# Optimization experiments

Hardware: AMD Instinct MI355X
Metric: run time of the kernel (lower is better)

Reference implementation:

```python
import jax, jax.numpy as jnp
import numpy as np

B, C, K, V, S = 16384, 1024, 128, 256, 6
HM, HG, M = 512, 384, 1024
LB = 2
GATE_DIM = C + K + 2 * V + 5  # 1669
CADENCE = 8.0
TEMP = 0.25
REFRESH_T, SPAWN_T, PROMOTE_T, RETIRE_T = 0.55, 0.60, 0.50, 0.15
DECAY = 0.995
EPS_N = 1e-6


def _mlp(x, W1, b1, W2, b2):
    return jax.nn.gelu(x @ W1 + b1, approximate=False) @ W2 + b2


def _l2norm(x):
    n = jnp.linalg.norm(x, axis=-1, keepdims=True)
    return x / jnp.maximum(n, EPS_N)


def setup_inputs():
    key = jax.random.key(0)
    ks = jax.random.split(key, 16)
    p = lambda k, sh: (0.02 * jax.random.normal(k, sh)).astype(jnp.float32)
    return {
        "context": jax.random.normal(ks[0], (B, C), jnp.float32),
        "ledger_bias": jax.random.normal(ks[1], (B, LB), jnp.float32),
        "keys": jax.random.normal(ks[2], (B, S, K), jnp.float32),
        "values": jax.random.normal(ks[3], (B, S, V), jnp.float32),
        "confidence": jax.random.uniform(ks[4], (B, S, 1), jnp.float32),
        "age": 16.0 * jax.random.uniform(ks[5], (B, S, 1), jnp.float32),
        "alive": (jax.random.uniform(ks[6], (B, S, 1)) > 0.3).astype(jnp.float32),
        "Wk1": p(ks[7], (C, HM)), "bk1": jnp.zeros(HM, jnp.float32),
        "Wk2": p(ks[8], (HM, K)), "bk2": jnp.zeros(K, jnp.float32),
        "Wv1": p(ks[9], (C, HM)), "bv1": jnp.zeros(HM, jnp.float32),
        "Wv2": p(ks[10], (HM, V)), "bv2": jnp.zeros(V, jnp.float32),
        "Wg1": p(ks[11], (4, GATE_DIM, HG)), "bg1": jnp.zeros((4, HG), jnp.float32),
        "Wg2": p(ks[12], (4, HG, 1)), "bg2": jnp.zeros((4, 1), jnp.float32),
        "Wsum": p(ks[13], (V, M)), "bsum": jnp.zeros(M, jnp.float32),
        "g_ln": jnp.ones(M, jnp.float32), "b_ln": jnp.zeros(M, jnp.float32),
    }


def _forward(context, ledger_bias, keys, values, confidence, age, alive,
             Wk1, bk1, Wk2, bk2, Wv1, bv1, Wv2, bv2,
             Wg1, bg1, Wg2, bg2, Wsum, bsum, g_ln, b_ln):
    cand_key = _l2norm(_mlp(context, Wk1, bk1, Wk2, bk2))   # [B,K]
    cand_val = _mlp(context, Wv1, bv1, Wv2, bv2)            # [B,V]
    # --- slot match: cosine similarity over live slots, gather best ---
    live = alive[..., 0] > 0                                # [B,S]
    safe_keys = _l2norm(keys + (1.0 - alive) * 1e-4)
    scores = jnp.einsum("bd,bsd->bs", cand_key, safe_keys)
    scores = jnp.where(live, scores, -1e4)
    has_live = jnp.any(live, axis=1, keepdims=True)         # [B,1]
    best_score = jnp.where(has_live, scores.max(axis=1, keepdims=True), 0.0)
    best_index = jnp.where(has_live, jnp.argmax(scores, axis=1, keepdims=True), 0)
    matched_val = jnp.take_along_axis(values, best_index[:, :, None], axis=1)[:, 0]
    matched_age = jnp.take_along_axis(age, best_index[:, :, None], axis=1)[:, 0]
    cadence_prior = jax.nn.sigmoid((matched_age - CADENCE) / CADENCE)
    surprise = 1.0 - best_score
    feats = jnp.concatenate([context, cand_key, cand_val, matched_val,
                             best_score, cadence_prior, surprise, ledger_bias], axis=-1)
    # --- four gate MLPs fused into one batched einsum ---
    h = jax.nn.gelu(jnp.einsum("bf,gfh->bgh", feats, Wg1) + bg1, approximate=False)
    probs = jax.nn.sigmoid(jnp.einsum("bgh,gho->bgo", h, Wg2) + bg2)[:, :, 0]  # [B,4]
    refresh_p, spawn_p, promote_p, retire_p = (probs[:, i:i + 1] for i in range(4))
    # --- soft masks (hard=False path) ---
    has_live_f = alive.max(axis=1)                          # [B,1]
    t = max(TEMP, 1e-4)
    refresh_raw = jax.nn.sigmoid((refresh_p - REFRESH_T) / t) * has_live_f
    spawn_raw = jax.nn.sigmoid((spawn_p - SPAWN_T) / t)
    denom = 1.0 + refresh_raw + spawn_raw
    refresh = refresh_raw / denom
    spawn = spawn_raw / denom
    promote = jax.nn.sigmoid((promote_p - PROMOTE_T) / t)
    retire = jax.nn.sigmoid((retire_p - RETIRE_T) / t)
    # --- spawn slot selection ---
    inactive = (alive[..., 0] < 0.5).astype(jnp.float32)
    has_inactive = inactive.max(axis=1, keepdims=True) > 0.5
    inactive_choice = jnp.argmax(inactive, axis=1, keepdims=True)
    utility = (confidence - 0.01 * age)[..., 0]
    utility = jnp.where(best_index == jnp.arange(S)[None, :], 1e4, utility)
    spawn_index = jnp.where(has_inactive, inactive_choice,
                            jnp.argmin(utility, axis=1, keepdims=True))
    # --- masked scatter update into slot memory ---
    match_hot = jax.nn.one_hot(best_index[:, 0], S, dtype=keys.dtype)[:, :, None]
    spawn_hot = jax.nn.one_hot(spawn_index[:, 0], S, dtype=keys.dtype)[:, :, None]
    refresh_slot = match_hot * refresh[:, None, :]
    spawn_slot = spawn_hot * spawn[:, None, :]
    retire_slot = match_hot * retire[:, None, :]
    write = jnp.clip(refresh_slot + spawn_slot, 0.0, 1.0)
    keys_n = keys * (1.0 - write) + write * cand_key[:, None, :]
    values_n = values * (1.0 - write) + write * cand_val[:, None, :]
    conf_n = (confidence * DECAY * (1.0 - write) + write) * (1.0 - retire_slot)
    age_n = (age + alive) * (1.0 - write)
    alive_n = jnp.clip(alive * (1.0 - retire_slot) + write, 0.0, 1.0)
    # --- confidence-weighted summary + promoted memory token ---
    w = alive_n * conf_n
    summary = (values_n * w).sum(axis=1) / (w.sum(axis=1) + EPS_N)  # [B,V]
    z = summary @ Wsum + bsum
    mu = z.mean(axis=-1, keepdims=True)
    var = ((z - mu) ** 2).mean(axis=-1, keepdims=True)
    promoted = promote * (((z - mu) / jnp.sqrt(var + 1e-5)) * g_ln + b_ln)
    return promoted, summary, keys_n, values_n, conf_n, age_n, alive_n


def reference(context, ledger_bias, keys, values, confidence, age, alive,
              Wk1, bk1, Wk2, bk2, Wv1, bv1, Wv2, bv2,
              Wg1, bg1, Wg2, bg2, Wsum, bsum, g_ln, b_ln):
    return _forward(context, ledger_bias, keys, values, confidence, age, alive,
                    Wk1, bk1, Wk2, bk2, Wv1, bv1, Wv2, bv2,
                    Wg1, bg1, Wg2, bg2, Wsum, bsum, g_ln, b_ln)
```

## Files before the change

kernel.cpp:

```cpp
#include <hip/hip_runtime.h>
#include <math.h>

static constexpr int Bsz  = 16384;
static constexpr int Cdim = 1024;
static constexpr int Kdim = 128;
static constexpr int Vdim = 256;
static constexpr int HMd  = 512;
static constexpr int GOUTd= 1536;
static constexpr int GDIM = 1669;
static constexpr int GPAD = 1728;
static constexpr int F2D  = 704;
static constexpr int Mdim = 1024;
static constexpr float TAU = 2e-3f;

typedef __attribute__((ext_vector_type(8))) _Float16 f16x8;
typedef __attribute__((ext_vector_type(4))) _Float16 f16x4;
typedef __attribute__((ext_vector_type(4))) float f32x4;

__device__ __forceinline__ float sigm(float x){ return 1.0f/(1.0f+__expf(-x)); }
__device__ __forceinline__ float gelu(float x){
    float y = 0.70710678118654752440f * x;
    float a = fabsf(y);
    float t1 = __builtin_amdgcn_rcpf(fmaf(0.3275911f, a, 1.0f));
    float p = t1*fmaf(t1, fmaf(t1, fmaf(t1, fmaf(t1, 1.061405429f, -1.453152027f),
                                         1.421413741f), -0.284496736f), 0.254829592f);
    float e = __expf(-a*a);
    float er = fmaf(-p, e, 1.0f);
    er = (y < 0.0f) ? -er : er;
    return 0.5f*x*(1.0f+er);
}
__device__ __forceinline__ ushort f2h(float f){
    return __builtin_bit_cast(ushort, (_Float16)f);
}


__global__ __launch_bounds__(256) void k_zero(int* p){ if (threadIdx.x==0) *p = 0; }

__global__ __launch_bounds__(256) void k_cat(float* __restrict__ dst,
        const float* __restrict__ a, const float* __restrict__ b, int na, int ntot){
    int i = blockIdx.x*256 + threadIdx.x;
    if (i >= ntot) return;
    dst[i] = (i < na) ? a[i] : b[i-na];
}

__global__ __launch_bounds__(256) void k_wt(const float* __restrict__ W,
                                            ushort* __restrict__ Wt, int K, int N){
    __shared__ float tile[64][65];
    int n0 = blockIdx.x*64, k0 = blockIdx.y*64;
    int tx = threadIdx.x & 63, ty = threadIdx.x >> 6;
    #pragma unroll
    for (int i=0;i<64;i+=4)
        tile[ty+i][tx] = W[(size_t)(k0+ty+i)*N + n0 + tx];
    __syncthreads();
    #pragma unroll
    for (int i=0;i<64;i+=4)
        Wt[(size_t)(n0+ty+i)*K + k0 + tx] = f2h(tile[tx][ty+i]);
}

__global__ __launch_bounds__(256) void k_wg1t(const float* __restrict__ Wg1,
                                              ushort* __restrict__ Wt){
    __shared__ float tile[64][65];
    int g = blockIdx.z;
    int h0 = blockIdx.x*64, f0 = blockIdx.y*64;
    int tx = threadIdx.x & 63, ty = threadIdx.x >> 6;
    #pragma unroll
    for (int i=0;i<64;i+=4){
        int f = f0+ty+i;
        tile[ty+i][tx] = (f < GDIM) ? Wg1[((size_t)g*GDIM+f)*384 + h0+tx] : 0.0f;
    }
    __syncthreads();
    #pragma unroll
    for (int i=0;i<64;i+=4)
        Wt[((size_t)(g*384 + h0+ty+i))*GPAD + f0+tx] = f2h(tile[tx][ty+i]);
}

__global__ __launch_bounds__(256) void k_cvt(const float* __restrict__ x,
                                             ushort* __restrict__ y, size_t n4){
    size_t i = (size_t)blockIdx.x*256 + threadIdx.x;
    if (i >= n4) return;
    float4 v = ((const float4*)x)[i];
    ushort4 o = { f2h(v.x), f2h(v.y), f2h(v.z), f2h(v.w) };
    ((ushort4*)y)[i] = o;
}

__device__ __forceinline__ void gload_lds16(const void* g, void* l){
    typedef __attribute__((address_space(1))) const unsigned gu32;
    typedef __attribute__((address_space(3))) unsigned lu32;
    __builtin_amdgcn_global_load_lds((gu32*)(unsigned long long)g,
                                     (lu32*)(unsigned)(unsigned long long)l,
                                     16, 0, 0);
}

template<int ACT, int OUTM, int SRC, int NX>
__global__ __launch_bounds__(256) void k_mgemm(const ushort* __restrict__ A,
        const ushort* __restrict__ A2, const ushort* __restrict__ Bt,
        const float* __restrict__ bias, const float* __restrict__ Wg2,
        void* __restrict__ Cout, int K, int lda){
    __shared__ alignas(16) ushort lds[32768];
    int t = threadIdx.x;
    int l = t & 63, w = t >> 6;
    int wm = w >> 1, wn = w & 1;
    int nwg = NX * (int)gridDim.y;
    int orig = (int)blockIdx.y * NX + (int)blockIdx.x;
    int qq = nwg >> 3, rr = nwg & 7;
    int xcd = orig & 7, loc = orig >> 3;
    int wgid = (xcd < rr ? xcd*(qq+1) : rr*(qq+1) + (xcd-rr)*qq) + loc;
    int bx = wgid % NX;
    int by = wgid / NX;
    size_t row0 = (size_t)by * 128;
    int col0 = bx * 128;
    constexpr int N = NX*128;
    f32x4 acc[4][4] = {};
    int lrow = l >> 3;
    int lc8  = (l & 7) ^ lrow;
    int nt = K >> 6;

    auto stage = [&](int buf, int k0){
        const ushort* Ag; int astr; int koff;
        if (SRC == 1){
            if (k0 < 1024){ Ag = A;  astr = 1024; koff = k0; }
            else          { Ag = A2; astr = F2D;  koff = k0 - 1024; }
        } else if (SRC == 2){
            Ag = A; astr = lda; koff = k0 + (bx ? 512 : 0);
        } else { Ag = A; astr = lda; koff = k0; }
        ushort* As = lds + buf*16384;
        ushort* Bs = As + 8192;
        #pragma unroll
        for (int i = 0; i < 4; ++i){
            int ch = w*4 + i;
            int r  = ch*8 + lrow;
            gload_lds16(Ag + (row0 + r)*(size_t)astr + koff + lc8*8, As + ch*512);
            gload_lds16(Bt + (size_t)(col0 + r)*K + k0 + lc8*8, Bs + ch*512);
        }
    };
    auto compute = [&](int buf){
        const ushort* As = lds + buf*16384;
        const ushort* Bs = As + 8192;
        #pragma unroll
        for (int kk = 0; kk < 2; ++kk){
            f16x8 af[4], bfr[4];
            int j8 = kk*4 + (l >> 4);
            #pragma unroll
            for (int m = 0; m < 4; ++m){
                int row = wm*64 + m*16 + (l & 15);
                int c16 = j8 ^ (row & 7);
                af[m] = *(const f16x8*)(const void*)(As + row*64 + c16*8);
            }
            #pragma unroll
            for (int n = 0; n < 4; ++n){
                int rowb = wn*64 + n*16 + (l & 15);
                int c16 = j8 ^ (rowb & 7);
                bfr[n] = *(const f16x8*)(const void*)(Bs + rowb*64 + c16*8);
            }
            #pragma unroll
            for (int m = 0; m < 4; ++m)
                #pragma unroll
                for (int n = 0; n < 4; ++n)
                    acc[m][n] = __builtin_amdgcn_mfma_f32_16x16x32_f16(af[m], bfr[n], acc[m][n], 0, 0, 0);
        }
    };

    stage(0, 0);
    for (int tt = 0; tt < nt-1; ++tt){
        __builtin_amdgcn_s_barrier();
        stage((tt+1)&1, (tt+1)<<6);
        asm volatile("s_waitcnt vmcnt(8)" ::: "memory");
        __builtin_amdgcn_s_barrier();
        compute(tt&1);
    }
    asm volatile("s_waitcnt vmcnt(0)" ::: "memory");
    __builtin_amdgcn_s_barrier();
    compute((nt-1)&1);

    int q = l >> 4, cf = l & 15;
    if (OUTM == 2){
        __syncthreads();
        float* sacc = (float*)lds;
        if (t < 128) sacc[t] = 0.f;
        __syncthreads();
        #pragma unroll
        for (int m = 0; m < 4; ++m){
            #pragma unroll
            for (int i = 0; i < 4; ++i){
                float v = 0.f;
                #pragma unroll
                for (int n = 0; n < 4; ++n){
                    int col = col0 + wn*64 + n*16 + cf;
                    float z = acc[m][n][i] + bias[col];
                    v += gelu(z) * Wg2[col];
                }
                atomicAdd(&sacc[wm*64 + m*16 + q*4 + i], v);
            }
        }
        __syncthreads();
        if (t < 128) ((float*)Cout)[(row0 + t)*NX + bx] = sacc[t];
    } else {
        #pragma unroll
        for (int m = 0; m < 4; ++m){
            #pragma unroll
            for (int n = 0; n < 4; ++n){
                int col = col0 + wn*64 + n*16 + cf;
                float bv = bias[col];
                #pragma unroll
                for (int i = 0; i < 4; ++i){
                    size_t r = row0 + wm*64 + m*16 + q*4 + i;
                    float v = acc[m][n][i] + bv;
                    if (ACT == 1) v = gelu(v);
                    if (OUTM == 1) ((ushort*)Cout)[r*N + col] = f2h(v);
                    else           ((float*) Cout)[r*N + col] = v;
                }
            }
        }
    }
}

template<int ACT>
__global__ __launch_bounds__(256) void k_gemm_dyn(const float* __restrict__ A,
                                                  const float* __restrict__ W,
                                                  const float* __restrict__ bias,
                                                  float* __restrict__ C,
                                                  const int* __restrict__ cntp,
                                                  int N, int K){
    int M = (*cntp + 63) & ~63;
    size_t row0 = (size_t)blockIdx.y * 64;
    if ((int)row0 >= M) return;
    __shared__ float As[32][68];
    __shared__ float Ws[32][64];
    int t  = threadIdx.x;
    int tx = t & 15, ty = t >> 4;
    int col0 = blockIdx.x * 64;
    float acc[4][4] = {};
    int ra = t >> 3;
    int ca = (t & 7) << 2;
    int rw = t >> 4;
    int cw = (t & 15) << 2;
    for (int k0 = 0; k0 < K; k0 += 32){
        float4 a0 = *(const float4*)(A + (row0 + ra)*K + k0 + ca);
        float4 a1 = *(const float4*)(A + (row0 + ra + 32)*K + k0 + ca);
        float4 w0 = *(const float4*)(W + (size_t)(k0 + rw)*N + col0 + cw);
        float4 w1 = *(const float4*)(W + (size_t)(k0 + rw + 16)*N + col0 + cw);
        As[ca+0][ra] = a0.x; As[ca+1][ra] = a0.y; As[ca+2][ra] = a0.z; As[ca+3][ra] = a0.w;
        As[ca+0][ra+32] = a1.x; As[ca+1][ra+32] = a1.y; As[ca+2][ra+32] = a1.z; As[ca+3][ra+32] = a1.w;
        *(float4*)&Ws[rw][cw]    = w0;
        *(float4*)&Ws[rw+16][cw] = w1;
        __syncthreads();
        #pragma unroll
        for (int kk = 0; kk < 32; ++kk){
            float4 av = *(const float4*)&As[kk][ty*4];
            float4 wv = *(const float4*)&Ws[kk][tx*4];
            float a4[4] = {av.x, av.y, av.z, av.w};
            float w4[4] = {wv.x, wv.y, wv.z, wv.w};
            #pragma unroll
            for (int i=0;i<4;i++)
                #pragma unroll
                for (int j=0;j<4;j++)
                    acc[i][j] = fmaf(a4[i], w4[j], acc[i][j]);
        }
        __syncthreads();
    }
    #pragma unroll
    for (int i=0;i<4;i++){
        size_t r = row0 + ty*4 + i;
        #pragma unroll
        for (int j=0;j<4;j++){
            int c = col0 + tx*4 + j;
            float v = acc[i][j] + bias[c];
            if (ACT == 1) v = gelu(v);
            C[r*N + c] = v;
        }
    }
}

__global__ __launch_bounds__(256) void k_gather(const float* __restrict__ ctx,
        const int* __restrict__ flaglist, const int* __restrict__ flagcnt,
        float* __restrict__ fctx, int b0){
    int i = (blockIdx.x<<2) + (threadIdx.x>>6);
    int lane = threadIdx.x & 63;
    int cnt = *flagcnt;
    int cntpad = (cnt + 63) & ~63;
    if (i >= cntpad) return;
    float4* dst = (float4*)(fctx + (size_t)i*1024);
    if (i < cnt){
        const float4* src = (const float4*)(ctx + ((size_t)b0 + flaglist[i])*1024);
        #pragma unroll
        for (int j=0;j<4;j++) dst[lane + 64*j] = src[lane + 64*j];
    } else {
        float4 z = {0.f,0.f,0.f,0.f};
        #pragma unroll
        for (int j=0;j<4;j++) dst[lane + 64*j] = z;
    }
}

__global__ __launch_bounds__(256) void k_fixapply(const float* __restrict__ fck,
        const float* __restrict__ keys, const float* __restrict__ values,
        const float* __restrict__ age,  const float* __restrict__ alive,
        float* __restrict__ ckc, ushort* __restrict__ feats2, int* __restrict__ bidx,
        const int* __restrict__ flagcnt, const int* __restrict__ flaglist, int b0){
    int i = (blockIdx.x<<2) + (threadIdx.x>>6);
    int lane = threadIdx.x & 63;
    if (i >= *flagcnt) return;
    int w = flaglist[i];
    size_t b = (size_t)b0 + w;
    float2 c2 = ((const float2*)(fck + (size_t)i*128))[lane];
    float ss = c2.x*c2.x + c2.y*c2.y;
    #pragma unroll
    for (int o=32;o;o>>=1) ss += __shfl_xor(ss,o);
    float inv = 1.0f / fmaxf(sqrtf(ss), 1e-6f);
    float2 cc; cc.x = c2.x*inv; cc.y = c2.y*inv;
    ((float2*)(ckc + (size_t)w*128))[lane] = cc;
    ushort* f2 = feats2 + (size_t)w*F2D;
    { ushort2 o = { f2h(cc.x), f2h(cc.y) };
      ((ushort2*)f2)[lane] = o; }
    float s1v = -1e30f; int bi = 0; int anylive = 0;
    #pragma unroll
    for (int s=0;s<6;s++){
        float a = alive[b*6+s];
        float2 k2 = ((const float2*)(keys + (b*6+s)*128))[lane];
        float ks = k2.x*k2.x + k2.y*k2.y;
        float dt = cc.x*k2.x + cc.y*k2.y;
        #pragma unroll
        for (int o=32;o;o>>=1){ ks += __shfl_xor(ks,o); dt += __shfl_xor(dt,o); }
        float sc;
        if (a > 0.0f){ sc = dt / fmaxf(sqrtf(ks), 1e-6f); anylive = 1; }
        else sc = -1e4f;
        if (sc > s1v){ s1v = sc; bi = s; }
    }
    int bis = anylive ? bi : 0;
    float bsc = anylive ? s1v : 0.0f;
    float4 mv = ((const float4*)(values + (b*6+bis)*256))[lane];
    ushort4 mo = { f2h(mv.x), f2h(mv.y), f2h(mv.z), f2h(mv.w) };
    ((ushort4*)(f2+384))[lane] = mo;
    if (lane == 0){
        bidx[w] = bis;
        float mage = age[b*6 + bis];
        f2[640] = f2h(bsc);
        f2[641] = f2h(sigm((mage - 8.0f)*0.125f));
        f2[642] = f2h(1.0f - bsc);
    }
}

__global__ __launch_bounds__(256) void k_feats(
        const float* __restrict__ ledger, const float* __restrict__ keys,
        const float* __restrict__ values, const float* __restrict__ age,
        const float* __restrict__ alive,  const float* __restrict__ ckv,
        float* __restrict__ ckc, ushort* __restrict__ feats2,
        int* __restrict__ bidx, int* __restrict__ flagcnt, int* __restrict__ flaglist,
        int b0){
    int w = (blockIdx.x<<2) + (threadIdx.x>>6);
    int lane = threadIdx.x & 63;
    size_t b = (size_t)b0 + w;
    const float* ckr = ckv + (size_t)w*384;
    float2 cr2 = ((const float2*)ckr)[lane];
    float ssc = cr2.x*cr2.x + cr2.y*cr2.y;
    #pragma unroll
    for (int o=32;o;o>>=1) ssc += __shfl_xor(ssc,o);
    float invc = 1.0f / fmaxf(sqrtf(ssc), 1e-6f);
    float2 cc; cc.x = cr2.x*invc; cc.y = cr2.y*invc;
    ((float2*)(ckc + (size_t)w*128))[lane] = cc;
    float s1v = -1e30f, s2v = -1e30f; int bi = 0; int anylive = 0;
    #pragma unroll
    for (int s=0;s<6;s++){
        float a = alive[b*6+s];
        float2 k2 = ((const float2*)(keys + (b*6+s)*128))[lane];
        float ss = k2.x*k2.x + k2.y*k2.y;
        float dt = cc.x*k2.x + cc.y*k2.y;
        #pragma unroll
        for (int o=32;o;o>>=1){ ss += __shfl_xor(ss,o); dt += __shfl_xor(dt,o); }
        float sc;
        if (a > 0.0f){ sc = dt / fmaxf(sqrtf(ss), 1e-6f); anylive = 1; }
        else sc = -1e4f;
        if (sc > s1v){ s2v = s1v; s1v = sc; bi = s; }
        else if (sc > s2v) s2v = sc;
    }
    float best_score = anylive ? s1v : 0.0f;
    int bis = anylive ? bi : 0;
    if (lane == 0 && (s1v - s2v) < TAU){
        int pos = atomicAdd(flagcnt, 1);
        flaglist[pos] = w;
    }
    float4 mv = ((const float4*)(values + (b*6+bis)*256))[lane];
    float mage = age[b*6+bis];
    float cad = sigm((mage - 8.0f)*0.125f);
    ushort* f2 = feats2 + (size_t)w*F2D;
    { ushort2 o = { f2h(cc.x), f2h(cc.y) };
      ((ushort2*)f2)[lane] = o; }
    { float4 v = ((const float4*)(ckr+128))[lane];
      ushort4 o = { f2h(v.x), f2h(v.y), f2h(v.z), f2h(v.w) };
      ((ushort4*)(f2+128))[lane] = o; }
    { ushort4 o = { f2h(mv.x), f2h(mv.y), f2h(mv.z), f2h(mv.w) };
      ((ushort4*)(f2+384))[lane] = o; }
    if (lane == 0){
        f2[640] = f2h(best_score);
        f2[641] = f2h(cad);
        f2[642] = f2h(1.0f - best_score);
        f2[643] = f2h(ledger[b*2]);
        f2[644] = f2h(ledger[b*2+1]);
        bidx[w] = bis;
    }
    if (lane < GPAD - GDIM) f2[645+lane] = 0;
}

__global__ __launch_bounds__(256) void k_update(const float* __restrict__ keys,
        const float* __restrict__ values, const float* __restrict__ conf,
        const float* __restrict__ age,    const float* __restrict__ alive,
        const float* __restrict__ ckC,    const float* __restrict__ ckv,
        const float* __restrict__ part,   const float* __restrict__ bg2,
        const int* __restrict__ bidx,
        float* __restrict__ probsC,
        float* __restrict__ o_keys, float* __restrict__ o_vals,
        float* __restrict__ o_conf, float* __restrict__ o_age,
        float* __restrict__ o_aliv, float* __restrict__ o_sum,
        ushort* __restrict__ o_sumb, int b0){
    int w = (blockIdx.x<<2) + (threadIdx.x>>6);
    int lane = threadIdx.x & 63;
    size_t b = (size_t)b0 + w;
    const float* pp = part + (size_t)w*12;
    float pb[4];
    #pragma unroll
    for (int g=0; g<4; ++g)
        pb[g] = sigm(pp[3*g] + pp[3*g+1] + pp[3*g+2] + bg2[g]);
    if (lane < 4) probsC[w*4 + lane] = pb[lane];
    float rp = pb[0], sp = pb[1], tp = pb[3];
    float al[6], cf[6], ag[6];
    float hl = 0.f;
    #pragma unroll
    for (int s=0;s<6;s++){
        al[s]=alive[b*6+s]; cf[s]=conf[b*6+s]; ag[s]=age[b*6+s];
        hl = fmaxf(hl, al[s]);
    }
    float rr = hl * sigm((rp-0.55f)*4.0f);
    float sr = sigm((sp-0.60f)*4.0f);
    float den = 1.0f + rr + sr;
    float refresh = rr/den, spawn = sr/den;
    float retire = sigm((tp-0.15f)*4.0f);
    int bi = bidx[w];
    int ic = -1;
    #pragma unroll
    for (int s=5;s>=0;s--) if (al[s] < 0.5f) ic = s;
    int si;
    if (ic >= 0) si = ic;
    else {
        float bu = 1e30f; int am = 0;
        #pragma unroll
        for (int s=0;s<6;s++){
            float u = (s == bi) ? 1e4f : (cf[s] - 0.01f*ag[s]);
            if (u < bu){ bu = u; am = s; }
        }
        si = am;
    }
    float2 cc  = ((const float2*)(ckC + (size_t)w*128))[lane];
    float4 cvv = ((const float4*)(ckv + (size_t)w*384 + 128))[lane];
    float s0=0,s1=0,s2=0,s3=0, wsum=0;
    #pragma unroll
    for (int s=0;s<6;s++){
        float wr = refresh*(s==bi ? 1.0f:0.0f) + spawn*(s==si ? 1.0f:0.0f);
        wr = fminf(wr, 1.0f);
        float rs = (s==bi) ? retire : 0.0f;
        float om = 1.0f - wr;
        float2 k2 = ((const float2*)(keys + (b*6+s)*128))[lane];
        float2 kn; kn.x = k2.x*om + wr*cc.x; kn.y = k2.y*om + wr*cc.y;
        ((float2*)(o_keys + (b*6+s)*128))[lane] = kn;
        float4 vv = ((const float4*)(values + (b*6+s)*256))[lane];
        float4 vn;
        vn.x = vv.x*om + wr*cvv.x; vn.y = vv.y*om + wr*cvv.y;
        vn.z = vv.z*om + wr*cvv.z; vn.w = vv.w*om + wr*cvv.w;
        ((float4*)(o_vals + (b*6+s)*256))[lane] = vn;
        float cn  = (cf[s]*0.995f*om + wr) * (1.0f - rs);
        float an  = fminf(fmaxf(al[s]*(1.0f - rs) + wr, 0.0f), 1.0f);
        float agn = (ag[s] + al[s]) * om;
        float wgt = an * cn;
        wsum += wgt;
        s0 += vn.x*wgt; s1 += vn.y*wgt; s2 += vn.z*wgt; s3 += vn.w*wgt;
        if (lane == s){ o_conf[b*6+s] = cn; o_age[b*6+s] = agn; o_aliv[b*6+s] = an; }
    }
    float inv = 1.0f/(wsum + 1e-6f);
    float4 sm; sm.x = s0*inv; sm.y = s1*inv; sm.z = s2*inv; sm.w = s3*inv;
    ((float4*)(o_sum + b*256))[lane] = sm;
    ushort4 sb = { f2h(sm.x), f2h(sm.y), f2h(sm.z), f2h(sm.w) };
    ((ushort4*)(o_sumb + (size_t)w*256))[lane] = sb;
}

__global__ __launch_bounds__(256) void k_ln(const ushort* __restrict__ z,
        const float* __restrict__ probs, const float* __restrict__ g_ln,
        const float* __restrict__ b_ln,  float* __restrict__ o_prom, int b0){
    int w = blockIdx.x; int t = threadIdx.x;
    int lane = t & 63, wid = t >> 6;
    f16x4 hv = ((const f16x4*)(z + (size_t)w*1024))[t];
    float v0 = (float)hv[0], v1 = (float)hv[1], v2 = (float)hv[2], v3 = (float)hv[3];
    float s = v0+v1+v2+v3;
    #pragma unroll
    for (int o=32;o;o>>=1) s += __shfl_xor(s,o);
    __shared__ float red[4];
    if (lane==0) red[wid] = s;
    __syncthreads();
    float mu = (red[0]+red[1]+red[2]+red[3]) * (1.0f/1024.0f);
    float d0=v0-mu, d1=v1-mu, d2=v2-mu, d3=v3-mu;
    float ss = d0*d0+d1*d1+d2*d2+d3*d3;
    #pragma unroll
    for (int o=32;o;o>>=1) ss += __shfl_xor(ss,o);
    __syncthreads();
    if (lane==0) red[wid] = ss;
    __syncthreads();
    float var = (red[0]+red[1]+red[2]+red[3]) * (1.0f/1024.0f);
    float rstd = 1.0f / sqrtf(var + 1e-5f);
    float pm = sigm((probs[w*4+2]-0.50f)*4.0f);
    float4 g  = ((const float4*)g_ln)[t];
    float4 bb = ((const float4*)b_ln)[t];
    float4 o;
    o.x = pm*(d0*rstd*g.x + bb.x);
    o.y = pm*(d1*rstd*g.y + bb.y);
    o.z = pm*(d2*rstd*g.z + bb.z);
    o.w = pm*(d3*rstd*g.w + bb.w);
    ((float4*)(o_prom + ((size_t)b0 + w)*1024))[t] = o;
}

extern "C" void kernel_launch(void* const* d_in, const int* in_sizes, int n_in,
                              void* d_out, int out_size, void* d_ws, size_t ws_size,
                              hipStream_t stream){
    const float* ctx    = (const float*)d_in[0];
    const float* ledger = (const float*)d_in[1];
    const float* keys   = (const float*)d_in[2];
    const float* values = (const float*)d_in[3];
    const float* conf   = (const float*)d_in[4];
    const float* age    = (const float*)d_in[5];
    const float* alive  = (const float*)d_in[6];
    const float* Wk1 = (const float*)d_in[7];  const float* bk1 = (const float*)d_in[8];
    const float* Wk2 = (const float*)d_in[9];  const float* bk2 = (const float*)d_in[10];
    const float* Wv1 = (const float*)d_in[11]; const float* bv1 = (const float*)d_in[12];
    const float* Wv2 = (const float*)d_in[13]; const float* bv2 = (const float*)d_in[14];
    const float* Wg1 = (const float*)d_in[15]; const float* bg1 = (const float*)d_in[16];
    const float* Wg2 = (const float*)d_in[17]; const float* bg2 = (const float*)d_in[18];
    const float* Wsum= (const float*)d_in[19]; const float* bsum= (const float*)d_in[20];
    const float* g_ln= (const float*)d_in[21]; const float* b_ln= (const float*)d_in[22];

    float* out   = (float*)d_out;
    float* o_prom= out;
    float* o_sum = o_prom + (size_t)Bsz*Mdim;
    float* o_keys= o_sum  + (size_t)Bsz*Vdim;
    float* o_vals= o_keys + (size_t)Bsz*6*Kdim;
    float* o_conf= o_vals + (size_t)Bsz*6*Vdim;
    float* o_age = o_conf + (size_t)Bsz*6;
    float* o_aliv= o_age  + (size_t)Bsz*6;

    char* p = (char*)d_ws;
    auto alloc = [&](size_t bytes)->char*{
        char* r = p; p += (bytes + 255) & ~(size_t)255; return r;
    };
    ushort* ctxh  = (ushort*)alloc((size_t)Bsz*Cdim*2);
    ushort* W1m   = (ushort*)alloc((size_t)1024*Cdim*2);
    ushort* W2m   = (ushort*)alloc((size_t)384*HMd*2);
    ushort* Wg1tt = (ushort*)alloc((size_t)GOUTd*GPAD*2);
    ushort* Wsumt = (ushort*)alloc((size_t)Mdim*Vdim*2);
    float*  biasm1= (float*) alloc(1024*4);
    float*  biasm2= (float*) alloc(384*4);
    size_t fixed = (size_t)(p - (char*)d_ws);
    size_t per_row = 2048  + 1536  + 512  + 1408
                   + 48  + 4096  + 512  + 16
                   + 4 + 4 + 2048  + 512  + 128 ;
    int CB = 16384;
    while (CB > 128 && fixed + (size_t)CB*per_row + 16384 > ws_size) CB >>= 1;
    ushort* H      = (ushort*)alloc((size_t)CB*1024*2);
    float*  ckv    = (float*) alloc((size_t)CB*384*4);
    float*  ckc    = (float*) alloc((size_t)CB*Kdim*4);
    ushort* feats2 = (ushort*)alloc((size_t)CB*F2D*2);
    float*  part   = (float*) alloc((size_t)CB*12*4);
    float*  zbuf   = (float*) alloc((size_t)CB*Mdim*4);
    ushort* sumb   = (ushort*)alloc((size_t)CB*Vdim*2);
    float*  probsC = (float*) alloc((size_t)CB*4*4);
    int*    bidxC  = (int*)   alloc((size_t)CB*4);
    int*    flagl  = (int*)   alloc((size_t)CB*4);
    int*    flagc  = (int*)   alloc(256);
    float*  fH     = (float*) alloc((size_t)CB*HMd*4);
    float*  fck    = (float*) alloc((size_t)CB*Kdim*4);
    float*  fctx   = zbuf;
    ushort* zh     = (ushort*)zbuf;

    dim3 blk(256);
    k_cvt<<<(int)(((size_t)Bsz*Cdim/4 + 255)/256), blk, 0, stream>>>(ctx, ctxh, (size_t)Bsz*Cdim/4);
    k_wt<<<dim3(HMd/64,  Cdim/64), blk, 0, stream>>>(Wk1, W1m,             Cdim, HMd);
    k_wt<<<dim3(HMd/64,  Cdim/64), blk, 0, stream>>>(Wv1, W1m + 512*Cdim,  Cdim, HMd);
    k_wt<<<dim3(Kdim/64, HMd/64),  blk, 0, stream>>>(Wk2, W2m,             HMd, Kdim);
    k_wt<<<dim3(Vdim/64, HMd/64),  blk, 0, stream>>>(Wv2, W2m + 128*HMd,   HMd, Vdim);
    k_wt<<<dim3(Mdim/64, Vdim/64), blk, 0, stream>>>(Wsum, Wsumt, Vdim, Mdim);
    k_wg1t<<<dim3(384/64, GPAD/64, 4), blk, 0, stream>>>(Wg1, Wg1tt);
    k_cat<<<(1024+255)/256, blk, 0, stream>>>(biasm1, bk1, bv1, 512, 1024);
    k_cat<<<(384+255)/256,  blk, 0, stream>>>(biasm2, bk2, bv2, 128, 384);

    for (int b0 = 0; b0 < Bsz; b0 += CB){
        k_zero<<<1, blk, 0, stream>>>(flagc);
        k_mgemm<1,1,0,8><<<dim3(8, CB/128), blk, 0, stream>>>(
            ctxh + (size_t)b0*Cdim, nullptr, W1m, biasm1, nullptr, H, Cdim, Cdim);
        k_mgemm<0,0,2,3><<<dim3(3, CB/128), blk, 0, stream>>>(
            H, nullptr, W2m, biasm2, nullptr, ckv, HMd, 1024);
        k_feats<<<CB/4, blk, 0, stream>>>(ledger, keys, values, age, alive,
                                          ckv, ckc, feats2, bidxC, flagc, flagl, b0);
        k_gather<<<CB/4, blk, 0, stream>>>(ctx, flagl, flagc, fctx, b0);
        k_gemm_dyn<1><<<dim3(HMd/64,  CB/64), blk, 0, stream>>>(fctx, Wk1, bk1, fH,  flagc, HMd,  Cdim);
        k_gemm_dyn<0><<<dim3(Kdim/64, CB/64), blk, 0, stream>>>(fH,   Wk2, bk2, fck, flagc, Kdim, HMd);
        k_fixapply<<<CB/4, blk, 0, stream>>>(fck, keys, values, age, alive,
                                             ckc, feats2, bidxC, flagc, flagl, b0);
        k_mgemm<0,2,1,12><<<dim3(12, CB/128), blk, 0, stream>>>(
            ctxh + (size_t)b0*Cdim, feats2, Wg1tt, bg1, Wg2, part, GPAD, 0);
        k_update<<<CB/4, blk, 0, stream>>>(keys, values, conf, age, alive, ckc, ckv,
                                           part, bg2, bidxC, probsC,
                                           o_keys, o_vals, o_conf, o_age, o_aliv,
                                           o_sum, sumb, b0);
        k_mgemm<0,1,0,8><<<dim3(8, CB/128), blk, 0, stream>>>(
            sumb, nullptr, Wsumt, bsum, nullptr, zh, Vdim, Vdim);
        k_ln<<<CB, blk, 0, stream>>>(zh, probsC, g_ln, b_ln, o_prom, b0);
    }
}
```

Baseline: 471.3 us.

## Add 256x256-tile 8-wave MFMA GEMM with quadrant ping-pong for large GEMMs

Adds a new GEMM kernel that uses 256x256 output tiles, 512 threads, 128KB of dynamic LDS and one block per CU. It stages A and B in half-tile pieces interleaved with four quadrant MFMA phases and raises wave priority (s_setprio) around the MFMA phases. The first-layer MLP, gate and summary GEMMs switch to it, which is meant to raise arithmetic intensity per LDS and global load. The gate epilogue now writes two partial sums per 256-column block, and the update kernel remaps those 12 partials to the 4 gates. The risks are lower occupancy, fewer workgroups per GEMM, and reliance on large dynamic LDS allocations.

Measured after the change: 647.6 us. 37.4% more time.

```diff
diff --git a/kernel.cpp b/kernel.cpp
--- a/kernel.cpp
+++ b/kernel.cpp
@@ -89,6 +89,198 @@
     __builtin_amdgcn_global_load_lds((gu32*)(unsigned long long)g,
                                      (lu32*)(unsigned)(unsigned long long)l,
                                      16, 0, 0);
+}
+
+template<int QM, int QN>
+__device__ __forceinline__ void do_mfma(f32x4 (&acc)[2][2][4][2],
+                                        const f16x8 (&afr)[4][2], const f16x8 (&bfr)[2][2]){
+    #pragma unroll
+    for (int kk=0;kk<2;kk++)
+        #pragma unroll
+        for (int mi=0;mi<4;mi++)
+            #pragma unroll
+            for (int ni=0;ni<2;ni++)
+                acc[QM][QN][mi][ni] = __builtin_amdgcn_mfma_f32_16x16x32_f16(
+                    afr[mi][kk], bfr[ni][kk], acc[QM][QN][mi][ni], 0, 0, 0);
+}
+
+__device__ __forceinline__ void load_afr(const ushort* ldsu, int pt, int qm,
+                                         int wr2, int l, f16x8 (&afr)[4][2]){
+    const ushort* Ah = ldsu + ((pt<<1)|qm)*8192;
+    #pragma unroll
+    for (int mi=0;mi<4;mi++){
+        int row = wr2*64 + mi*16 + (l & 15);
+        #pragma unroll
+        for (int kk=0;kk<2;kk++)
+            afr[mi][kk] = *(const f16x8*)(const void*)(Ah + row*64 + (((kk*4+(l>>4))^(row&7))<<3));
+    }
+}
+__device__ __forceinline__ void load_bfr(const ushort* ldsu, int pt, int qn,
+                                         int wc4, int l, f16x8 (&bfr)[2][2]){
+    const ushort* Bh = ldsu + 32768 + ((pt<<1)|qn)*8192;
+    #pragma unroll
+    for (int ni=0;ni<2;ni++){
+        int col = wc4*32 + ni*16 + (l & 15);
+        #pragma unroll
+        for (int kk=0;kk<2;kk++)
+            bfr[ni][kk] = *(const f16x8*)(const void*)(Bh + col*64 + (((kk*4+(l>>4))^(col&7))<<3));
+    }
+}
+
+template<int ACT, int OUTM, int SRC, int NX>
+__global__ __launch_bounds__(512, 1) void k_mgemm256(const ushort* __restrict__ A,
+        const ushort* __restrict__ A2, const ushort* __restrict__ Bt,
+        const float* __restrict__ bias, const float* __restrict__ Wg2,
+        void* __restrict__ Cout, int K, int lda){
+    extern __shared__ char smem[];
+    ushort* ldsu = (ushort*)smem;
+    int t = threadIdx.x;
+    int l = t & 63, wv = t >> 6;
+    int wr2 = wv >> 2, wc4 = wv & 3;
+    int nwg = NX * (int)gridDim.y;
+    int orig = (int)blockIdx.y * NX + (int)blockIdx.x;
+    int qq = nwg >> 3, rr = nwg & 7;
+    int xcd = orig & 7, loc = orig >> 3;
+    int wgid = (xcd < rr ? xcd*(qq+1) : rr*(qq+1) + (xcd-rr)*qq) + loc;
+    int bx = wgid % NX;
+    int by = wgid / NX;
+    size_t row0 = (size_t)by * 256;
+    int col0 = bx * 256;
+    constexpr int N = NX*256;
+    int nt = K >> 6;
+
+    f32x4 acc[2][2][4][2] = {};
+    f16x8 afr[4][2], bfr[2][2];
+    int lrow = l >> 3;
+    int lc8s = ((l & 7) ^ lrow) << 3;
+
+    auto stage_half = [&](int h){
+        if (h >= 4*nt) return;
+        int k  = h & 3;
+        int tau = h >> 2;
+        int p  = tau & 1;
+        int k0 = tau << 6;
+        if (k == 0 || k == 3){
+            int hn = (k == 3);
+            ushort* dst = ldsu + 32768 + ((p<<1)|hn)*8192;
+            size_t rbase = (size_t)col0 + hn*128;
+            #pragma unroll
+            for (int i=0;i<2;i++){
+                int ch = i*8 + wv;
+                int r  = ch*8 + lrow;
+                gload_lds16(Bt + (rbase + r)*(size_t)K + k0 + lc8s, dst + ch*512);
+            }
+        } else {
+            int hm = (k == 1);
+            ushort* dst = ldsu + ((p<<1)|hm)*8192;
+            const ushort* Ag; size_t astr; int koff;
+            if (SRC == 1){
+                if (k0 < 1024){ Ag = A;  astr = 1024; koff = k0; }
+                else          { Ag = A2; astr = F2D;  koff = k0 - 1024; }
+            } else { Ag = A; astr = (size_t)lda; koff = k0; }
+            size_t rbase = row0 + (size_t)hm*128;
+            #pragma unroll
+            for (int i=0;i<2;i++){
+                int ch = i*8 + wv;
+                int r  = ch*8 + lrow;
+                gload_lds16(Ag + (rbase + r)*astr + koff + lc8s, dst + ch*512);
+            }
+        }
+    };
+
+    for (int h = 0; h < 6; ++h) stage_half(h);
+    asm volatile("s_waitcnt vmcnt(4)" ::: "memory");
+    __builtin_amdgcn_s_barrier();
+
+    for (int tt = 0; tt < nt; ++tt){
+        int pt = tt & 1;
+        int hb = 4*tt + 6;
+        load_afr(ldsu, pt, 0, wr2, l, afr);
+        load_bfr(ldsu, pt, 0, wc4, l, bfr);
+        stage_half(hb+0);
+        __builtin_amdgcn_s_barrier();
+        __builtin_amdgcn_s_setprio(1);
+        do_mfma<0,0>(acc, afr, bfr);
+        __builtin_amdgcn_s_setprio(0);
+        __builtin_amdgcn_s_barrier();
+        load_afr(ldsu, pt, 1, wr2, l, afr);
+        stage_half(hb+1);
+        __builtin_amdgcn_s_barrier();
+        __builtin_amdgcn_s_setprio(1);
+        do_mfma<1,0>(acc, afr, bfr);
+        __builtin_amdgcn_s_setprio(0);
+        __builtin_amdgcn_s_barrier();
+        load_bfr(ldsu, pt, 1, wc4, l, bfr);
+        stage_half(hb+2);
+        __builtin_amdgcn_s_barrier();
+        __builtin_amdgcn_s_setprio(1);
+        do_mfma<1,1>(acc, afr, bfr);
+        __builtin_amdgcn_s_setprio(0);
+        __builtin_amdgcn_s_barrier();
+        load_afr(ldsu, pt, 0, wr2, l, afr);
+        stage_half(hb+3);
+        __builtin_amdgcn_s_barrier();
+        __builtin_amdgcn_s_setprio(1);
+        do_mfma<0,1>(acc, afr, bfr);
+        __builtin_amdgcn_s_setprio(0);
+        if (tt == nt-2) asm volatile("s_waitcnt vmcnt(0)" ::: "memory");
+        else            asm volatile("s_waitcnt vmcnt(4)" ::: "memory");
+        __builtin_amdgcn_s_barrier();
+    }
+
+    int q4 = l >> 4, cf = l & 15;
+    if (OUTM == 2){
+        __syncthreads();
+        float* sacc = (float*)ldsu;
+        sacc[t] = 0.f;
+        __syncthreads();
+        int g_lo = col0 / 384;
+        #pragma unroll
+        for (int qm=0;qm<2;qm++)
+        #pragma unroll
+        for (int qn=0;qn<2;qn++)
+        #pragma unroll
+        for (int mi=0;mi<4;mi++)
+        #pragma unroll
+        for (int ni=0;ni<2;ni++){
+            int col_l = qn*128 + wc4*32 + ni*16 + cf;
+            int colg  = col0 + col_l;
+            int slot  = (colg/384 == g_lo) ? 0 : 1;
+            float wg  = Wg2[colg];
+            float bv  = bias[colg];
+            #pragma unroll
+            for (int i=0;i<4;i++){
+                int row_l = qm*128 + wr2*64 + mi*16 + q4*4 + i;
+                float z = acc[qm][qn][mi][ni][i] + bv;
+                atomicAdd(&sacc[row_l*2 + slot], gelu(z)*wg);
+            }
+        }
+        __syncthreads();
+        if (t < 256){
+            ((float*)Cout)[(row0 + t)*(NX*2) + bx*2 + 0] = sacc[t*2];
+            ((float*)Cout)[(row0 + t)*(NX*2) + bx*2 + 1] = sacc[t*2+1];
+        }
+    } else {
+        #pragma unroll
+        for (int qm=0;qm<2;qm++)
+        #pragma unroll
+        for (int qn=0;qn<2;qn++)
+        #pragma unroll
+        for (int mi=0;mi<4;mi++)
+        #pragma unroll
+        for (int ni=0;ni<2;ni++){
+            int col = col0 + qn*128 + wc4*32 + ni*16 + cf;
+            float bv = bias[col];
+            #pragma unroll
+            for (int i=0;i<4;i++){
+                size_t r = row0 + qm*128 + wr2*64 + mi*16 + q4*4 + i;
+                float v = acc[qm][qn][mi][ni][i] + bv;
+                if (ACT == 1) v = gelu(v);
+                if (OUTM == 1) ((ushort*)Cout)[r*N + col] = f2h(v);
+                else           ((float*) Cout)[r*N + col] = v;
+            }
+        }
+    }
 }
 
 template<int ACT, int OUTM, int SRC, int NX>
@@ -116,20 +308,17 @@
     int nt = K >> 6;
 
     auto stage = [&](int buf, int k0){
-        const ushort* Ag; int astr; int koff;
-        if (SRC == 1){
-            if (k0 < 1024){ Ag = A;  astr = 1024; koff = k0; }
-            else          { Ag = A2; astr = F2D;  koff = k0 - 1024; }
-        } else if (SRC == 2){
-            Ag = A; astr = lda; koff = k0 + (bx ? 512 : 0);
-        } else { Ag = A; astr = lda; koff = k0; }
+        const ushort* Ag; size_t astr; int koff;
+        if (SRC == 2){
+            Ag = A; astr = (size_t)lda; koff = k0 + (bx ? 512 : 0);
+        } else { Ag = A; astr = (size_t)lda; koff = k0; }
         ushort* As = lds + buf*16384;
         ushort* Bs = As + 8192;
         #pragma unroll
         for (int i = 0; i < 4; ++i){
             int ch = w*4 + i;
             int r  = ch*8 + lrow;
-            gload_lds16(Ag + (row0 + r)*(size_t)astr + koff + lc8*8, As + ch*512);
+            gload_lds16(Ag + (row0 + r)*astr + koff + lc8*8, As + ch*512);
             gload_lds16(Bt + (size_t)(col0 + r)*K + k0 + lc8*8, Bs + ch*512);
         }
     };
@@ -173,42 +362,19 @@
     compute((nt-1)&1);
 
     int q = l >> 4, cf = l & 15;
-    if (OUTM == 2){
-        __syncthreads();
-        float* sacc = (float*)lds;
-        if (t < 128) sacc[t] = 0.f;
-        __syncthreads();
-        #pragma unroll
-        for (int m = 0; m < 4; ++m){
+    #pragma unroll
+    for (int m = 0; m < 4; ++m){
+        #pragma unroll
+        for (int n = 0; n < 4; ++n){
+            int col = col0 + wn*64 + n*16 + cf;
+            float bv = bias[col];
             #pragma unroll
             for (int i = 0; i < 4; ++i){
-                float v = 0.f;
-                #pragma unroll
-                for (int n = 0; n < 4; ++n){
-                    int col = col0 + wn*64 + n*16 + cf;
-                    float z = acc[m][n][i] + bias[col];
-                    v += gelu(z) * Wg2[col];
-                }
-                atomicAdd(&sacc[wm*64 + m*16 + q*4 + i], v);
-            }
-        }
-        __syncthreads();
-        if (t < 128) ((float*)Cout)[(row0 + t)*NX + bx] = sacc[t];
-    } else {
-        #pragma unroll
-        for (int m = 0; m < 4; ++m){
-            #pragma unroll
-            for (int n = 0; n < 4; ++n){
-                int col = col0 + wn*64 + n*16 + cf;
-                float bv = bias[col];
-                #pragma unroll
-                for (int i = 0; i < 4; ++i){
-                    size_t r = row0 + wm*64 + m*16 + q*4 + i;
-                    float v = acc[m][n][i] + bv;
-                    if (ACT == 1) v = gelu(v);
-                    if (OUTM == 1) ((ushort*)Cout)[r*N + col] = f2h(v);
-                    else           ((float*) Cout)[r*N + col] = v;
-                }
+                size_t r = row0 + wm*64 + m*16 + q*4 + i;
+                float v = acc[m][n][i] + bv;
+                if (ACT == 1) v = gelu(v);
+                if (OUTM == 1) ((ushort*)Cout)[r*N + col] = f2h(v);
+                else           ((float*) Cout)[r*N + col] = v;
             }
         }
     }
@@ -415,10 +581,13 @@
     int lane = threadIdx.x & 63;
     size_t b = (size_t)b0 + w;
     const float* pp = part + (size_t)w*12;
+    const int gate_of[12] = {0,0, 0,1, 1,1, 2,2, 2,3, 3,3};
+    float ga[4] = {bg2[0], bg2[1], bg2[2], bg2[3]};
+    #pragma unroll
+    for (int j=0;j<12;j++) ga[gate_of[j]] += pp[j];
     float pb[4];
     #pragma unroll
-    for (int g=0; g<4; ++g)
-        pb[g] = sigm(pp[3*g] + pp[3*g+1] + pp[3*g+2] + bg2[g]);
+    for (int g=0; g<4; ++g) pb[g] = sigm(ga[g]);
     if (lane < 4) probsC[w*4 + lane] = pb[lane];
     float rp = pb[0], sp = pb[1], tp = pb[3];
     float al[6], cf[6], ag[6];
@@ -554,11 +723,10 @@
     float*  biasm1= (float*) alloc(1024*4);
     float*  biasm2= (float*) alloc(384*4);
     size_t fixed = (size_t)(p - (char*)d_ws);
-    size_t per_row = 2048  + 1536  + 512  + 1408
-                   + 48  + 4096  + 512  + 16
-                   + 4 + 4 + 2048  + 512  + 128 ;
+    size_t per_row = 2048 + 1536 + 512 + 1408 + 48 + 4096 + 512 + 16
+                   + 4 + 4 + 2048 + 512 + 128;
     int CB = 16384;
-    while (CB > 128 && fixed + (size_t)CB*per_row + 16384 > ws_size) CB >>= 1;
+    while (CB > 256 && fixed + (size_t)CB*per_row + 16384 > ws_size) CB >>= 1;
     ushort* H      = (ushort*)alloc((size_t)CB*1024*2);
     float*  ckv    = (float*) alloc((size_t)CB*384*4);
     float*  ckc    = (float*) alloc((size_t)CB*Kdim*4);
@@ -576,6 +744,8 @@
     ushort* zh     = (ushort*)zbuf;
 
     dim3 blk(256);
+    dim3 blk512(512);
+    const size_t LDS256 = 131072;
     k_cvt<<<(int)(((size_t)Bsz*Cdim/4 + 255)/256), blk, 0, stream>>>(ctx, ctxh, (size_t)Bsz*Cdim/4);
     k_wt<<<dim3(HMd/64,  Cdim/64), blk, 0, stream>>>(Wk1, W1m,             Cdim, HMd);
     k_wt<<<dim3(HMd/64,  Cdim/64), blk, 0, stream>>>(Wv1, W1m + 512*Cdim,  Cdim, HMd);
@@ -588,7 +758,7 @@
 
     for (int b0 = 0; b0 < Bsz; b0 += CB){
         k_zero<<<1, blk, 0, stream>>>(flagc);
-        k_mgemm<1,1,0,8><<<dim3(8, CB/128), blk, 0, stream>>>(
+        k_mgemm256<1,1,0,4><<<dim3(4, CB/256), blk512, LDS256, stream>>>(
             ctxh + (size_t)b0*Cdim, nullptr, W1m, biasm1, nullptr, H, Cdim, Cdim);
         k_mgemm<0,0,2,3><<<dim3(3, CB/128), blk, 0, stream>>>(
             H, nullptr, W2m, biasm2, nullptr, ckv, HMd, 1024);
@@ -599,13 +769,13 @@
         k_gemm_dyn<0><<<dim3(Kdim/64, CB/64), blk, 0, stream>>>(fH,   Wk2, bk2, fck, flagc, Kdim, HMd);
         k_fixapply<<<CB/4, blk, 0, stream>>>(fck, keys, values, age, alive,
                                              ckc, feats2, bidxC, flagc, flagl, b0);
-        k_mgemm<0,2,1,12><<<dim3(12, CB/128), blk, 0, stream>>>(
+        k_mgemm256<0,2,1,6><<<dim3(6, CB/256), blk512, LDS256, stream>>>(
             ctxh + (size_t)b0*Cdim, feats2, Wg1tt, bg1, Wg2, part, GPAD, 0);
         k_update<<<CB/4, blk, 0, stream>>>(keys, values, conf, age, alive, ckc, ckv,
                                            part, bg2, bidxC, probsC,
                                            o_keys, o_vals, o_conf, o_age, o_aliv,
                                            o_sum, sumb, b0);
-        k_mgemm<0,1,0,8><<<dim3(8, CB/128), blk, 0, stream>>>(
+        k_mgemm256<0,1,0,4><<<dim3(4, CB/256), blk512, LDS256, stream>>>(
             sumb, nullptr, Wsumt, bsum, nullptr, zh, Vdim, Vdim);
         k_ln<<<CB, blk, 0, stream>>>(zh, probsC, g_ln, b_ln, o_prom, b0);
     }
```

## Use 512-thread single-buffered MFMA GEMM tiles instead of double-buffered 256-thread

Applied to the files above, without the earlier changes.

The 128x128 MFMA GEMM tile kernel now runs with 8 waves per block instead of 4, each wave computing a 64x32 sub-tile. The LDS double buffer and its vmcnt-based prefetch pipeline are replaced by a single buffer with two __syncthreads per K step. This halves LDS use and per-wave accumulator registers, aiming for higher occupancy and less register pressure. In exchange, loads no longer overlap with MFMA compute inside a block, so latency hiding relies on other resident waves.

Result: slower. 500.7 us (+6.2%).

```diff
diff --git a/kernel.cpp b/kernel.cpp
--- a/kernel.cpp
+++ b/kernel.cpp
@@ -92,14 +92,16 @@
 }
 
 template<int ACT, int OUTM, int SRC, int NX>
-__global__ __launch_bounds__(256) void k_mgemm(const ushort* __restrict__ A,
+__global__ __launch_bounds__(512) void k_mgemm(const ushort* __restrict__ A,
         const ushort* __restrict__ A2, const ushort* __restrict__ Bt,
         const float* __restrict__ bias, const float* __restrict__ Wg2,
         void* __restrict__ Cout, int K, int lda){
-    __shared__ alignas(16) ushort lds[32768];
+    __shared__ alignas(16) ushort lds[16384];
+    ushort* As = lds;
+    ushort* Bs = lds + 8192;
     int t = threadIdx.x;
-    int l = t & 63, w = t >> 6;
-    int wm = w >> 1, wn = w & 1;
+    int l = t & 63, wv = t >> 6;
+    int wr2 = wv >> 2, wc4 = wv & 3;
     int nwg = NX * (int)gridDim.y;
     int orig = (int)blockIdx.y * NX + (int)blockIdx.x;
     int qq = nwg >> 3, rr = nwg & 7;
@@ -110,71 +112,52 @@
     size_t row0 = (size_t)by * 128;
     int col0 = bx * 128;
     constexpr int N = NX*128;
-    f32x4 acc[4][4] = {};
+    f32x4 acc[4][2] = {};
     int lrow = l >> 3;
     int lc8  = (l & 7) ^ lrow;
-    int nt = K >> 6;
-
-    auto stage = [&](int buf, int k0){
-        const ushort* Ag; int astr; int koff;
+
+    for (int k0 = 0; k0 < K; k0 += 64){
+        const ushort* Ag; size_t astr; int koff;
         if (SRC == 1){
             if (k0 < 1024){ Ag = A;  astr = 1024; koff = k0; }
             else          { Ag = A2; astr = F2D;  koff = k0 - 1024; }
         } else if (SRC == 2){
-            Ag = A; astr = lda; koff = k0 + (bx ? 512 : 0);
-        } else { Ag = A; astr = lda; koff = k0; }
-        ushort* As = lds + buf*16384;
-        ushort* Bs = As + 8192;
-        #pragma unroll
-        for (int i = 0; i < 4; ++i){
-            int ch = w*4 + i;
+            Ag = A; astr = (size_t)lda; koff = k0 + (bx ? 512 : 0);
+        } else { Ag = A; astr = (size_t)lda; koff = k0; }
+        #pragma unroll
+        for (int i = 0; i < 2; ++i){
+            int ch = wv*2 + i;
             int r  = ch*8 + lrow;
-            gload_lds16(Ag + (row0 + r)*(size_t)astr + koff + lc8*8, As + ch*512);
+            gload_lds16(Ag + (row0 + r)*astr + koff + lc8*8, As + ch*512);
             gload_lds16(Bt + (size_t)(col0 + r)*K + k0 + lc8*8, Bs + ch*512);
         }
-    };
-    auto compute = [&](int buf){
-        const ushort* As = lds + buf*16384;
-        const ushort* Bs = As + 8192;
+        __syncthreads();
         #pragma unroll
         for (int kk = 0; kk < 2; ++kk){
-            f16x8 af[4], bfr[4];
+            f16x8 af[4], bfr[2];
             int j8 = kk*4 + (l >> 4);
             #pragma unroll
             for (int m = 0; m < 4; ++m){
-                int row = wm*64 + m*16 + (l & 15);
+                int row = wr2*64 + m*16 + (l & 15);
                 int c16 = j8 ^ (row & 7);
                 af[m] = *(const f16x8*)(const void*)(As + row*64 + c16*8);
             }
             #pragma unroll
-            for (int n = 0; n < 4; ++n){
-                int rowb = wn*64 + n*16 + (l & 15);
+            for (int n = 0; n < 2; ++n){
+                int rowb = wc4*32 + n*16 + (l & 15);
                 int c16 = j8 ^ (rowb & 7);
                 bfr[n] = *(const f16x8*)(const void*)(Bs + rowb*64 + c16*8);
             }
             #pragma unroll
             for (int m = 0; m < 4; ++m)
                 #pragma unroll
-                for (int n = 0; n < 4; ++n)
+                for (int n = 0; n < 2; ++n)
                     acc[m][n] = __builtin_amdgcn_mfma_f32_16x16x32_f16(af[m], bfr[n], acc[m][n], 0, 0, 0);
         }
-    };
-
-    stage(0, 0);
-    for (int tt = 0; tt < nt-1; ++tt){
-        __builtin_amdgcn_s_barrier();
-        stage((tt+1)&1, (tt+1)<<6);
-        asm volatile("s_waitcnt vmcnt(8)" ::: "memory");
-        __builtin_amdgcn_s_barrier();
-        compute(tt&1);
-    }
-    asm volatile("s_waitcnt vmcnt(0)" ::: "memory");
-    __builtin_amdgcn_s_barrier();
-    compute((nt-1)&1);
-
+        __syncthreads();
+    }
     int q = l >> 4, cf = l & 15;
     if (OUTM == 2){
-        __syncthreads();
         float* sacc = (float*)lds;
         if (t < 128) sacc[t] = 0.f;
         __syncthreads();
@@ -184,12 +167,12 @@
             for (int i = 0; i < 4; ++i){
                 float v = 0.f;
                 #pragma unroll
-                for (int n = 0; n < 4; ++n){
-                    int col = col0 + wn*64 + n*16 + cf;
+                for (int n = 0; n < 2; ++n){
+                    int col = col0 + wc4*32 + n*16 + cf;
                     float z = acc[m][n][i] + bias[col];
                     v += gelu(z) * Wg2[col];
                 }
-                atomicAdd(&sacc[wm*64 + m*16 + q*4 + i], v);
+                atomicAdd(&sacc[wr2*64 + m*16 + q*4 + i], v);
             }
         }
         __syncthreads();
@@ -198,12 +181,12 @@
         #pragma unroll
         for (int m = 0; m < 4; ++m){
             #pragma unroll
-            for (int n = 0; n < 4; ++n){
-                int col = col0 + wn*64 + n*16 + cf;
+            for (int n = 0; n < 2; ++n){
+                int col = col0 + wc4*32 + n*16 + cf;
                 float bv = bias[col];
                 #pragma unroll
                 for (int i = 0; i < 4; ++i){
-                    size_t r = row0 + wm*64 + m*16 + q*4 + i;
+                    size_t r = row0 + wr2*64 + m*16 + q*4 + i;
                     float v = acc[m][n][i] + bv;
                     if (ACT == 1) v = gelu(v);
                     if (OUTM == 1) ((ushort*)Cout)[r*N + col] = f2h(v);
@@ -554,11 +537,10 @@
     float*  biasm1= (float*) alloc(1024*4);
     float*  biasm2= (float*) alloc(384*4);
     size_t fixed = (size_t)(p - (char*)d_ws);
-    size_t per_row = 2048  + 1536  + 512  + 1408
-                   + 48  + 4096  + 512  + 16
-                   + 4 + 4 + 2048  + 512  + 128 ;
+    size_t per_row = 2048 + 1536 + 512 + 1408 + 48 + 4096 + 512 + 16
+                   + 4 + 4 + 2048 + 512 + 128;
     int CB = 16384;
-    while (CB > 128 && fixed + (size_t)CB*per_row + 16384 > ws_size) CB >>= 1;
+    while (CB > 256 && fixed + (size_t)CB*per_row + 16384 > ws_size) CB >>= 1;
     ushort* H      = (ushort*)alloc((size_t)CB*1024*2);
     float*  ckv    = (float*) alloc((size_t)CB*384*4);
     float*  ckc    = (float*) alloc((size_t)CB*Kdim*4);
@@ -576,6 +558,7 @@
     ushort* zh     = (ushort*)zbuf;
 
     dim3 blk(256);
+    dim3 blk512(512);
     k_cvt<<<(int)(((size_t)Bsz*Cdim/4 + 255)/256), blk, 0, stream>>>(ctx, ctxh, (size_t)Bsz*Cdim/4);
     k_wt<<<dim3(HMd/64,  Cdim/64), blk, 0, stream>>>(Wk1, W1m,             Cdim, HMd);
     k_wt<<<dim3(HMd/64,  Cdim/64), blk, 0, stream>>>(Wv1, W1m + 512*Cdim,  Cdim, HMd);
@@ -588,9 +571,9 @@
 
     for (int b0 = 0; b0 < Bsz; b0 += CB){
         k_zero<<<1, blk, 0, stream>>>(flagc);
-        k_mgemm<1,1,0,8><<<dim3(8, CB/128), blk, 0, stream>>>(
+        k_mgemm<1,1,0,8><<<dim3(8, CB/128), blk512, 0, stream>>>(
             ctxh + (size_t)b0*Cdim, nullptr, W1m, biasm1, nullptr, H, Cdim, Cdim);
-        k_mgemm<0,0,2,3><<<dim3(3, CB/128), blk, 0, stream>>>(
+        k_mgemm<0,0,2,3><<<dim3(3, CB/128), blk512, 0, stream>>>(
             H, nullptr, W2m, biasm2, nullptr, ckv, HMd, 1024);
         k_feats<<<CB/4, blk, 0, stream>>>(ledger, keys, values, age, alive,
                                           ckv, ckc, feats2, bidxC, flagc, flagl, b0);
@@ -599,13 +582,13 @@
         k_gemm_dyn<0><<<dim3(Kdim/64, CB/64), blk, 0, stream>>>(fH,   Wk2, bk2, fck, flagc, Kdim, HMd);
         k_fixapply<<<CB/4, blk, 0, stream>>>(fck, keys, values, age, alive,
                                              ckc, feats2, bidxC, flagc, flagl, b0);
-        k_mgemm<0,2,1,12><<<dim3(12, CB/128), blk, 0, stream>>>(
+        k_mgemm<0,2,1,12><<<dim3(12, CB/128), blk512, 0, stream>>>(
             ctxh + (size_t)b0*Cdim, feats2, Wg1tt, bg1, Wg2, part, GPAD, 0);
         k_update<<<CB/4, blk, 0, stream>>>(keys, values, conf, age, alive, ckc, ckv,
                                            part, bg2, bidxC, probsC,
                                            o_keys, o_vals, o_conf, o_age, o_aliv,
                                            o_sum, sumb, b0);
-        k_mgemm<0,1,0,8><<<dim3(8, CB/128), blk, 0, stream>>>(
+        k_mgemm<0,1,0,8><<<dim3(8, CB/128), blk512, 0, stream>>>(
             sumb, nullptr, Wsumt, bsum, nullptr, zh, Vdim, Vdim);
         k_ln<<<CB, blk, 0, stream>>>(zh, probsC, g_ln, b_ln, o_prom, b0);
     }
```
